# Kernel tuning notes

Hardware: AMD Instinct MI355X
Metric: run time of the kernel (lower is better)

## Reference

```python
import jax, jax.numpy as jnp
import numpy as np

NEG_INF = -9e15
ALPHA = 0.2  # LeakyReLU negative slope

N, IN_F, OUT_F = 8192, 512, 64


def setup_inputs() -> dict:
    key = jax.random.key(0)
    k1, k2, k3, k4 = jax.random.split(key, 4)
    input = jax.random.normal(k1, (N, IN_F), dtype=jnp.float32)
    adj = jax.random.randint(k2, (N, N), 0, 2, dtype=jnp.int32)
    init_range = float(np.sqrt(6.0 / (IN_F + OUT_F)))
    W = jax.random.uniform(k3, (IN_F, OUT_F), dtype=jnp.float32,
                           minval=-init_range, maxval=init_range)
    a_range = float(np.sqrt(6.0 / (2 * OUT_F + 1)))
    a = jax.random.uniform(k4, (2 * OUT_F, 1), dtype=jnp.float32,
                           minval=-a_range, maxval=a_range)
    return {"input": input, "adj": adj, "W": W, "a": a}


def reference(input, adj, W, a):
    h = input @ W                      # [N, F']
    a_left, a_right = a[:OUT_F], a[OUT_F:]   # each [F', 1]
    att_l = h @ a_left                 # [N, 1]
    att_r = h @ a_right                # [N, 1]
    e = jax.nn.leaky_relu(att_l + att_r.T, negative_slope=ALPHA)  # [N, N]
    e = jnp.where(adj == 0, jnp.float32(NEG_INF), e)
    attention = jax.nn.softmax(e, axis=1)
    # dropout is identity in eval mode (training=False)
    h_prime = attention @ h            # [N, F']
    return jax.nn.elu(h_prime)         # concat=True -> ELU activation
```

## Files before the change

kernel.cpp:

```cpp
#include <hip/hip_runtime.h>
#include <stdint.h>

#define ALPHA 0.2f
#define LOG2E 1.44269504088896340736f

typedef __attribute__((ext_vector_type(8))) short bf16x8;
typedef __attribute__((ext_vector_type(4))) float f32x4;

__device__ __forceinline__ unsigned short f2bf(float f) {
    unsigned u = __builtin_bit_cast(unsigned, f);
    u += 0x7fffu + ((u >> 16) & 1u);
    return (unsigned short)(u >> 16);
}
__device__ __forceinline__ float bf2f(unsigned short h) {
    unsigned u = ((unsigned)h) << 16;
    return __builtin_bit_cast(float, u);
}
__device__ __forceinline__ unsigned f2ord(float f) {
    unsigned b = __builtin_bit_cast(unsigned, f);
    return (b & 0x80000000u) ? ~b : (b | 0x80000000u);
}
__device__ __forceinline__ float ord2f(unsigned k) {
    unsigned b = (k & 0x80000000u) ? (k & 0x7fffffffu) : ~k;
    return __builtin_bit_cast(float, b);
}

__global__ __launch_bounds__(256) void gat_h(
    const float* __restrict__ input, const float* __restrict__ W,
    float* __restrict__ h)
{
    __shared__ float x_lds[16 * 128];
    const int tid = threadIdx.x;
    const int i0  = (blockIdx.x >> 2) * 16;
    const int k0  = (blockIdx.x & 3) * 128;

    {
        const int r  = tid >> 4;
        const int jc = (tid & 15) * 8;
        const float* src = input + (size_t)(i0 + r) * 512 + k0 + jc;
        *(f32x4*)&x_lds[r * 128 + jc]     = *(const f32x4*)src;
        *(f32x4*)&x_lds[r * 128 + jc + 4] = *(const f32x4*)(src + 4);
    }
    __syncthreads();

    const int c = tid & 63;
    const int w = tid >> 6;
    float acc[4] = {0.f, 0.f, 0.f, 0.f};
    const float* Wc = W + (size_t)k0 * 64 + c;
    #pragma unroll 4
    for (int kk = 0; kk < 128; kk += 4) {
        const float w0 = Wc[(kk+0)*64], w1 = Wc[(kk+1)*64];
        const float w2 = Wc[(kk+2)*64], w3 = Wc[(kk+3)*64];
        #pragma unroll
        for (int ri = 0; ri < 4; ++ri) {
            const f32x4 x = *(const f32x4*)&x_lds[(w + 4*ri) * 128 + kk];
            acc[ri] += x.x * w0 + x.y * w1 + x.z * w2 + x.w * w3;
        }
    }
    #pragma unroll
    for (int ri = 0; ri < 4; ++ri)
        unsafeAtomicAdd(&h[(size_t)(i0 + w + 4*ri) * 64 + c], acc[ri]);
}

__global__ __launch_bounds__(256) void gat_aux(
    const float* __restrict__ h, const float* __restrict__ a,
    float* __restrict__ attL, float* __restrict__ attR,
    unsigned short* __restrict__ hPack, unsigned* __restrict__ wsR)
{
    __shared__ float hl[32 * 64];
    __shared__ unsigned rmax;
    const int tid = threadIdx.x;
    const int j0  = blockIdx.x * 32;
    if (tid == 0) rmax = 0u;

    {
        const float* src = h + (size_t)j0 * 64 + tid * 8;
        *(f32x4*)&hl[tid * 8]     = *(const f32x4*)src;
        *(f32x4*)&hl[tid * 8 + 4] = *(const f32x4*)(src + 4);
    }
    __syncthreads();

    {
        const int row = tid >> 3;
        const int cs  = (tid & 7) * 8;
        float pL = 0.f, pR = 0.f;
        #pragma unroll
        for (int u = 0; u < 8; ++u) {
            const float hv = hl[row * 64 + cs + u];
            pL += hv * a[cs + u];
            pR += hv * a[64 + cs + u];
        }
        pL += __shfl_xor(pL, 1, 64); pR += __shfl_xor(pR, 1, 64);
        pL += __shfl_xor(pL, 2, 64); pR += __shfl_xor(pR, 2, 64);
        pL += __shfl_xor(pL, 4, 64); pR += __shfl_xor(pR, 4, 64);
        if ((tid & 7) == 0) {
            attL[j0 + row] = pL;
            attR[j0 + row] = pR;
            atomicMax(&rmax, f2ord(pR));
        }
    }

    {
        const int g = tid >> 6;
        const int l = tid & 63;
        const int m = l & 15;
        const int q = l >> 4;
        bf16x8 v;
        #pragma unroll
        for (int u = 0; u < 8; ++u)
            v[u] = (short)f2bf(hl[(q * 8 + u) * 64 + g * 16 + m]);
        *(bf16x8*)&hPack[(size_t)(blockIdx.x * 4 + g) * 512 + l * 8] = v;
    }

    __syncthreads();
    if (tid == 0) atomicMax(wsR, rmax);
}

__global__ __launch_bounds__(256) void gat_pack(
    const int* __restrict__ adj, unsigned* __restrict__ adjU)
{
    __shared__ unsigned char pk[4096];
    const int tid = threadIdx.x;
    const int ti  = blockIdx.x >> 2;
    const int jq  = blockIdx.x & 3;
    const int r   = tid >> 4;
    const int jo  = (tid & 15) * 8;
    const int lidx_base = ((tid & 3) * 16 + r) * 4 + ((tid & 15) >> 2);

    const int* src = adj + (size_t)(ti * 16 + r) * 8192 + jq * 2048 + jo;
    #pragma unroll 4
    for (int it = 0; it < 16; ++it) {
        const int4 v0 = *(const int4*)(src + it * 128);
        const int4 v1 = *(const int4*)(src + it * 128 + 4);
        unsigned b = 0;
        b |= (v0.x != 0) << 0; b |= (v0.y != 0) << 1;
        b |= (v0.z != 0) << 2; b |= (v0.w != 0) << 3;
        b |= (v1.x != 0) << 4; b |= (v1.y != 0) << 5;
        b |= (v1.z != 0) << 6; b |= (v1.w != 0) << 7;
        pk[it * 256 + lidx_base] = (unsigned char)b;
    }
    __syncthreads();
    const uint4 o = *(const uint4*)&pk[tid * 16];
    *(uint4*)((unsigned char*)adjU + ((size_t)ti * 64 + jq * 16) * 256 + tid * 16) = o;
}

__global__ __launch_bounds__(256, 8) void gat_attn(
    const unsigned* __restrict__ adjU,
    const float* __restrict__ attL, const float* __restrict__ attR,
    const unsigned short* __restrict__ hPack, const unsigned* __restrict__ wsR,
    float* __restrict__ outAcc, float* __restrict__ lAcc)
{
    __shared__ float acc_lds[4 * 64 * 16];
    __shared__ float l_lds[4 * 16];
    const int tid  = threadIdx.x;
    const int lane = tid & 63;
    const int wq   = tid >> 6;
    const int m    = lane & 15;
    const int quad = lane >> 4;
    const int ti   = blockIdx.x >> 2;
    const int q4   = blockIdx.x & 3;
    const int i0   = ti * 16;
    const int jc0  = q4 * 64 + wq * 16;

    const float R   = ord2f(*wsR);
    const float a_l = attL[i0 + m];
    const float t0  = a_l + R;
    const float M   = fmaxf(t0, ALPHA * t0);
    const float mc  = M * LOG2E;

    const unsigned*       ab_p = adjU + ((size_t)ti * 64 + (jc0 >> 2)) * 64 + lane;
    const float*          ar_p = attR + jc0 * 32 + quad * 8;
    const unsigned short* hp_p = hPack + (size_t)jc0 * 4 * 512 + lane * 8;

    f32x4 acc[4];
    #pragma unroll
    for (int g = 0; g < 4; ++g) acc[g] = (f32x4){0.f, 0.f, 0.f, 0.f};
    float lsum = 0.f;

    #pragma unroll
    for (int jg = 0; jg < 4; ++jg) {
        const unsigned ab = ab_p[jg * 64];
        #pragma unroll
        for (int t = 0; t < 4; ++t) {
            const int s = jg * 4 + t;
            const f32x4 r0 = *(const f32x4*)(ar_p + s * 32);
            const f32x4 r1 = *(const f32x4*)(ar_p + s * 32 + 4);
            bf16x8 B[4];
            #pragma unroll
            for (int g = 0; g < 4; ++g)
                B[g] = *(const bf16x8*)(hp_p + (size_t)(s * 4 + g) * 512);

            const unsigned bits = (ab >> (t * 8)) & 0xffu;
            const float tv[8] = { a_l + r0.x, a_l + r0.y, a_l + r0.z, a_l + r0.w,
                                  a_l + r1.x, a_l + r1.y, a_l + r1.z, a_l + r1.w };
            bf16x8 af;
            #pragma unroll
            for (int u = 0; u < 8; ++u) {
                const float e  = fmaxf(tv[u], ALPHA * tv[u]);
                const float pe = __builtin_amdgcn_exp2f(__builtin_fmaf(e, LOG2E, -mc));
                const float pv = (bits & (1u << u)) ? pe : 0.0f;
                const unsigned short pb = f2bf(pv);
                af[u] = (short)pb;
                lsum += bf2f(pb);
            }
            #pragma unroll
            for (int g = 0; g < 4; ++g)
                acc[g] = __builtin_amdgcn_mfma_f32_16x16x32_bf16(af, B[g], acc[g], 0, 0, 0);
        }
    }

    lsum += __shfl_xor(lsum, 16, 64);
    lsum += __shfl_xor(lsum, 32, 64);
    if (lane < 16) l_lds[wq * 16 + lane] = lsum;
    #pragma unroll
    for (int g = 0; g < 4; ++g)
        *(f32x4*)&acc_lds[(wq * 64 + lane) * 16 + g * 4] = acc[g];
    __syncthreads();

    #pragma unroll
    for (int q = 0; q < 4; ++q) {
        const int e      = tid + q * 256;
        const int lane_e = e >> 4;
        const int k16    = e & 15;
        float s = 0.f;
        #pragma unroll
        for (int ww = 0; ww < 4; ++ww) s += acc_lds[(ww * 64 + lane_e) * 16 + k16];
        const int row = (lane_e >> 4) * 4 + (k16 & 3);
        const int col = (k16 >> 2) * 16 + (lane_e & 15);
        unsafeAtomicAdd(&outAcc[(size_t)(i0 + row) * 64 + col], s);
    }
    if (tid < 16) {
        const float s = l_lds[tid] + l_lds[16 + tid] + l_lds[32 + tid] + l_lds[48 + tid];
        unsafeAtomicAdd(&lAcc[i0 + tid], s);
    }
}

__global__ __launch_bounds__(256) void gat_final(
    float* __restrict__ out, const float* __restrict__ lAcc)
{
    const int idx = blockIdx.x * 256 + threadIdx.x;
    const float v = out[idx] / lAcc[idx >> 6];
    out[idx] = v > 0.f ? v : (__builtin_amdgcn_exp2f(v * LOG2E) - 1.0f);
}

extern "C" void kernel_launch(void* const* d_in, const int* in_sizes, int n_in,
                              void* d_out, int out_size, void* d_ws, size_t ws_size,
                              hipStream_t stream) {
    const float* input = (const float*)d_in[0];
    const int*   adj   = (const int*)d_in[1];
    const float* W     = (const float*)d_in[2];
    const float* a     = (const float*)d_in[3];
    float* out = (float*)d_out;

    char* ws = (char*)d_ws;
    unsigned*       wsR   = (unsigned*)(ws + 0);
    float*          lAcc  = (float*)(ws + 4096);
    float*          h     = (float*)(ws + 36864);
    float*          attL  = (float*)(ws + 2134016);
    float*          attR  = (float*)(ws + 2166784);
    unsigned short* hPack = (unsigned short*)(ws + 2199552);
    unsigned*       adjU  = (unsigned*)(ws + 3248128);

    hipMemsetAsync(d_out, 0, (size_t)out_size * sizeof(float), stream);
    hipMemsetAsync(d_ws, 0, 2134016, stream);

    gat_pack <<<2048, 256, 0, stream>>>(adj, adjU);
    gat_h    <<<2048, 256, 0, stream>>>(input, W, h);
    gat_aux  <<< 256, 256, 0, stream>>>(h, a, attL, attR, hPack, wsR);
    gat_attn <<<2048, 256, 0, stream>>>(adjU, attL, attR, hPack, wsR, out, lAcc);
    gat_final<<<2048, 256, 0, stream>>>(out, lAcc);
}
```

Measured before the change: 443.1 us.

## Fuse adjacency bit-packing into attention kernel via shared memory

After: 415.4 us. 1.07x faster.

```diff
diff --git a/kernel.cpp b/kernel.cpp
--- a/kernel.cpp
+++ b/kernel.cpp
@@ -116,42 +116,14 @@
     if (tid == 0) atomicMax(wsR, rmax);
 }
 
-__global__ __launch_bounds__(256) void gat_pack(
-    const int* __restrict__ adj, unsigned* __restrict__ adjU)
-{
-    __shared__ unsigned char pk[4096];
-    const int tid = threadIdx.x;
-    const int ti  = blockIdx.x >> 2;
-    const int jq  = blockIdx.x & 3;
-    const int r   = tid >> 4;
-    const int jo  = (tid & 15) * 8;
-    const int lidx_base = ((tid & 3) * 16 + r) * 4 + ((tid & 15) >> 2);
-
-    const int* src = adj + (size_t)(ti * 16 + r) * 8192 + jq * 2048 + jo;
-    #pragma unroll 4
-    for (int it = 0; it < 16; ++it) {
-        const int4 v0 = *(const int4*)(src + it * 128);
-        const int4 v1 = *(const int4*)(src + it * 128 + 4);
-        unsigned b = 0;
-        b |= (v0.x != 0) << 0; b |= (v0.y != 0) << 1;
-        b |= (v0.z != 0) << 2; b |= (v0.w != 0) << 3;
-        b |= (v1.x != 0) << 4; b |= (v1.y != 0) << 5;
-        b |= (v1.z != 0) << 6; b |= (v1.w != 0) << 7;
-        pk[it * 256 + lidx_base] = (unsigned char)b;
-    }
-    __syncthreads();
-    const uint4 o = *(const uint4*)&pk[tid * 16];
-    *(uint4*)((unsigned char*)adjU + ((size_t)ti * 64 + jq * 16) * 256 + tid * 16) = o;
-}
-
 __global__ __launch_bounds__(256, 8) void gat_attn(
-    const unsigned* __restrict__ adjU,
+    const int* __restrict__ adj,
     const float* __restrict__ attL, const float* __restrict__ attR,
     const unsigned short* __restrict__ hPack, const unsigned* __restrict__ wsR,
     float* __restrict__ outAcc, float* __restrict__ lAcc)
 {
-    __shared__ float acc_lds[4 * 64 * 16];
-    __shared__ float l_lds[4 * 16];
+    __shared__ unsigned smem[4096];
+    __shared__ float l_lds[64];
     const int tid  = threadIdx.x;
     const int lane = tid & 63;
     const int wq   = tid >> 6;
@@ -162,13 +134,37 @@
     const int i0   = ti * 16;
     const int jc0  = q4 * 64 + wq * 16;
 
+    {
+        const int r    = tid >> 4;
+        const int lidx = (tid & 3) * 16 + r;
+        const int t    = (tid & 15) >> 2;
+        unsigned char* bb = (unsigned char*)smem;
+        const int* src = adj + (size_t)(i0 + r) * 8192 + q4 * 2048 + (tid & 15) * 8;
+        #pragma unroll 4
+        for (int it = 0; it < 16; ++it) {
+            const int4 v0 = *(const int4*)(src + it * 128);
+            const int4 v1 = *(const int4*)(src + it * 128 + 4);
+            unsigned b = 0;
+            b |= (v0.x != 0) << 0; b |= (v0.y != 0) << 1;
+            b |= (v0.z != 0) << 2; b |= (v0.w != 0) << 3;
+            b |= (v1.x != 0) << 4; b |= (v1.y != 0) << 5;
+            b |= (v1.z != 0) << 6; b |= (v1.w != 0) << 7;
+            bb[((((it >> 2) * 1024) + (it & 3) * 64 + lidx) << 2) + t] = (unsigned char)b;
+        }
+    }
+    __syncthreads();
+
+    unsigned abw[4];
+    #pragma unroll
+    for (int g4 = 0; g4 < 4; ++g4)
+        abw[g4] = smem[wq * 1024 + g4 * 64 + lane];
+
     const float R   = ord2f(*wsR);
     const float a_l = attL[i0 + m];
     const float t0  = a_l + R;
     const float M   = fmaxf(t0, ALPHA * t0);
     const float mc  = M * LOG2E;
 
-    const unsigned*       ab_p = adjU + ((size_t)ti * 64 + (jc0 >> 2)) * 64 + lane;
     const float*          ar_p = attR + jc0 * 32 + quad * 8;
     const unsigned short* hp_p = hPack + (size_t)jc0 * 4 * 512 + lane * 8;
 
@@ -179,7 +175,7 @@
 
     #pragma unroll
     for (int jg = 0; jg < 4; ++jg) {
-        const unsigned ab = ab_p[jg * 64];
+        const unsigned ab = abw[jg];
         #pragma unroll
         for (int t = 0; t < 4; ++t) {
             const int s = jg * 4 + t;
@@ -212,9 +208,10 @@
     lsum += __shfl_xor(lsum, 16, 64);
     lsum += __shfl_xor(lsum, 32, 64);
     if (lane < 16) l_lds[wq * 16 + lane] = lsum;
+    float* accf = (float*)smem;
     #pragma unroll
     for (int g = 0; g < 4; ++g)
-        *(f32x4*)&acc_lds[(wq * 64 + lane) * 16 + g * 4] = acc[g];
+        *(f32x4*)&accf[(wq * 64 + lane) * 16 + g * 4] = acc[g];
     __syncthreads();
 
     #pragma unroll
@@ -224,7 +221,7 @@
         const int k16    = e & 15;
         float s = 0.f;
         #pragma unroll
-        for (int ww = 0; ww < 4; ++ww) s += acc_lds[(ww * 64 + lane_e) * 16 + k16];
+        for (int ww = 0; ww < 4; ++ww) s += accf[(ww * 64 + lane_e) * 16 + k16];
         const int row = (lane_e >> 4) * 4 + (k16 & 3);
         const int col = (k16 >> 2) * 16 + (lane_e & 15);
         unsafeAtomicAdd(&outAcc[(size_t)(i0 + row) * 64 + col], s);
@@ -259,14 +256,12 @@
     float*          attL  = (float*)(ws + 2134016);
     float*          attR  = (float*)(ws + 2166784);
     unsigned short* hPack = (unsigned short*)(ws + 2199552);
-    unsigned*       adjU  = (unsigned*)(ws + 3248128);
 
     hipMemsetAsync(d_out, 0, (size_t)out_size * sizeof(float), stream);
     hipMemsetAsync(d_ws, 0, 2134016, stream);
 
-    gat_pack <<<2048, 256, 0, stream>>>(adj, adjU);
     gat_h    <<<2048, 256, 0, stream>>>(input, W, h);
     gat_aux  <<< 256, 256, 0, stream>>>(h, a, attL, attR, hPack, wsR);
-    gat_attn <<<2048, 256, 0, stream>>>(adjU, attL, attR, hPack, wsR, out, lAcc);
+    gat_attn <<<2048, 256, 0, stream>>>(adj, attL, attR, hPack, wsR, out, lAcc);
     gat_final<<<2048, 256, 0, stream>>>(out, lAcc);
 }
```
